# Kernel optimization log

Measured on AMD Instinct MI355X. Metric: run time of the kernel, lower is better.

The kernel has to match this reference:

```python
import jax, jax.numpy as jnp
import numpy as np

COST_COORDINATE = 1.0  # init kwarg cost_coordinate


def _lsa(cost):
    """Rectangular linear sum assignment (Jonker-Volgenant shortest augmenting
    path), matching scipy.optimize.linear_sum_assignment's algorithm/output.
    Returns (row_ind, col_ind) sorted by row_ind, length = min(nr, nc)."""
    cost = np.asarray(cost, dtype=np.float64)
    transposed = cost.shape[0] > cost.shape[1]
    if transposed:
        cost = cost.T
    nr, nc = cost.shape
    u = np.zeros(nr)
    v = np.zeros(nc)
    path = np.full(nc, -1, dtype=np.int64)
    col4row = np.full(nr, -1, dtype=np.int64)
    row4col = np.full(nc, -1, dtype=np.int64)
    for cur_row in range(nr):
        shortest = np.full(nc, np.inf)
        SR = np.zeros(nr, dtype=bool)
        SC = np.zeros(nc, dtype=bool)
        remaining = np.ones(nc, dtype=bool)
        min_val = 0.0
        i = cur_row
        sink = -1
        while sink == -1:
            SR[i] = True
            rem = np.nonzero(remaining)[0]
            cand = min_val + cost[i, rem] - u[i] - v[rem]
            better = cand < shortest[rem]
            idx_b = rem[better]
            shortest[idx_b] = cand[better]
            path[idx_b] = i
            j = rem[np.argmin(shortest[rem])]
            min_val = shortest[j]
            if not np.isfinite(min_val):
                raise RuntimeError('cost matrix is infeasible')
            SC[j] = True
            remaining[j] = False
            if row4col[j] == -1:
                sink = j
            else:
                i = row4col[j]
        # dual updates
        u[cur_row] += min_val
        mask = SR.copy()
        mask[cur_row] = False
        u[mask] += min_val - shortest[col4row[mask]]
        v[SC] -= min_val - shortest[SC]
        # augment along alternating path
        j = sink
        while True:
            i = path[j]
            row4col[j] = i
            col4row[i], j = j, col4row[i]
            if i == cur_row:
                break
    if transposed:
        order = np.argsort(col4row)
        return col4row[order], order.astype(np.int64)
    return np.arange(nr, dtype=np.int64), col4row


def setup_inputs() -> dict:
    key = jax.random.key(0)
    k1, k2 = jax.random.split(key)
    outputs = jax.random.uniform(k1, (16, 4096, 4), dtype=jnp.float32)  # [B, Q, 4]
    targets = jax.random.uniform(k2, (16, 128, 4), dtype=jnp.float32)   # [B, nt, 4]
    return {'outputs': outputs, 'targets': targets}


@jax.jit
def _cost_matrix(outputs, targets):
    # Block-diagonal part of torch.cdist(out.flatten(0,1), cat(targets), p=1):
    # only the per-image [Q, nt] blocks survive the .split(sizes, -1) in the
    # original, so we compute exactly those. C[b,q,t] = sum_d |out - tgt|.
    return COST_COORDINATE * jnp.abs(
        outputs[:, :, None, :] - targets[:, None, :, :]
    ).sum(-1)  # [B, Q, nt]


def reference(outputs, targets):
    C = _cost_matrix(outputs, targets)
    Cn = np.asarray(jax.device_get(C), dtype=np.float64)
    rows, cols = [], []
    for b in range(Cn.shape[0]):  # batch loop mirrors the original scipy loop
        r, c = _lsa(Cn[b])
        rows.append(r)
        cols.append(c)
    row_ind = jnp.asarray(np.stack(rows), dtype=jnp.int64)  # [B, min(Q,nt)]
    col_ind = jnp.asarray(np.stack(cols), dtype=jnp.int64)  # [B, min(Q,nt)]
    return C, row_ind, col_ind
```

## Files before the change

kernel.cpp:

```cpp
#include <hip/hip_runtime.h>
#include <math.h>

#define NB   16
#define NQ   4096
#define NTGT 128
#define CELEMS (NB * NQ * NTGT)

#define NSLOT 64
#define AT   512
#define ACPT 8
#define ANW  (AT / 64)

typedef unsigned long long u64;

__global__ __launch_bounds__(256) void cost_kernel(
    const float* __restrict__ outputs,
    const float* __restrict__ targets,
    float* __restrict__ C,
    u64*   __restrict__ rowkey2)
{
    __shared__ u64 part[4][NTGT];
    const int tid  = threadIdx.x;
    const int t4   = tid & 31;
    const int b    = blockIdx.x >> 6;
    const int blk  = blockIdx.x & (NSLOT - 1);
    const int idx0 = blockIdx.x * 2048 + tid;

    const float4* tg = reinterpret_cast<const float4*>(targets) + (b << 7) + (t4 << 2);
    float4 g[4];
    #pragma unroll
    for (int f = 0; f < 4; ++f) g[f] = tg[f];

    u64 keymin[4] = {~0ull, ~0ull, ~0ull, ~0ull};

    #pragma unroll
    for (int e = 0; e < 8; ++e) {
        int idx = idx0 + 256 * e;
        int bq  = idx >> 5;
        float4 o = reinterpret_cast<const float4*>(outputs)[bq];
        u64 q = (u64)(unsigned)(bq & (NQ - 1));
        float r[4];
        #pragma unroll
        for (int f = 0; f < 4; ++f) {
            float4 gg = g[f];
            r[f] = (fabsf(o.x - gg.x) + fabsf(o.y - gg.y)) +
                   (fabsf(o.z - gg.z) + fabsf(o.w - gg.w));
            u64 key = (((u64)__float_as_uint(r[f])) << 32) | q;
            if (key < keymin[f]) keymin[f] = key;
        }
        reinterpret_cast<float4*>(C)[idx] = make_float4(r[0], r[1], r[2], r[3]);
    }

    #pragma unroll
    for (int f = 0; f < 4; ++f) {
        u64 ov = __shfl_xor(keymin[f], 32);
        if (ov < keymin[f]) keymin[f] = ov;
    }
    if ((tid & 63) < 32) {
        int w = tid >> 6;
        #pragma unroll
        for (int f = 0; f < 4; ++f) part[w][(t4 << 2) + f] = keymin[f];
    }
    __syncthreads();

    if (tid < NTGT) {
        u64 k = part[0][tid];
        #pragma unroll
        for (int s = 1; s < 4; ++s) { u64 ov = part[s][tid]; if (ov < k) k = ov; }
        rowkey2[(((size_t)b * NSLOT) + blk) * NTGT + tid] = k;
    }
}

__global__ __launch_bounds__(AT, 1) void lsa_kernel(
    const float* __restrict__ outputs,
    const float* __restrict__ targets,
    const u64*   __restrict__ rowkey2,
    float* __restrict__ row_out,
    float* __restrict__ col_out)
{
    __shared__ double2 svp_[NQ];
    __shared__ unsigned claim_[NQ];
    __shared__ short  row4col_[NQ];
    __shared__ unsigned char path_[NQ];
    __shared__ float4 tgt_[NTGT];
    __shared__ double u_[NTGT];
    __shared__ u64    red2_[4][NTGT];
    __shared__ int    rowarg_[NTGT];
    __shared__ short  col4row_[NTGT];
    __shared__ short  left_[NTGT];
    __shared__ int    sc_j[NTGT];
    __shared__ double red_val[2][ANW];
    __shared__ int    red_idx[2][ANW];
    __shared__ u64    bmask_[2];

    const int tid = threadIdx.x;
    const int b   = blockIdx.x;
    const float4* outq = reinterpret_cast<const float4*>(outputs) + b * NQ;

    float4 o0 = outq[tid];
    float4 o1 = outq[tid + AT];
    float4 o2 = outq[tid + AT * 2];
    float4 o3 = outq[tid + AT * 3];
    float4 o4 = outq[tid + AT * 4];
    float4 o5 = outq[tid + AT * 5];
    float4 o6 = outq[tid + AT * 6];
    float4 o7 = outq[tid + AT * 7];

    #pragma unroll
    for (int kk = 0; kk < ACPT; ++kk) {
        int k = tid + AT * kk;
        svp_[k] = make_double2(0.0, 0.0);
        row4col_[k] = -1;
        claim_[k] = 0xFFFFFFFFu;
    }

    {
        const int t = tid & 127, s = tid >> 7;
        const u64* rk = rowkey2 + (size_t)b * NSLOT * NTGT;
        u64 k = ~0ull;
        #pragma unroll
        for (int gg = 0; gg < NSLOT / 4; ++gg) {
            u64 ov = rk[(s * (NSLOT / 4) + gg) * NTGT + t];
            if (ov < k) k = ov;
        }
        red2_[s][t] = k;
    }
    __syncthreads();

    if (tid < NTGT) {
        u64 key = red2_[0][tid];
        #pragma unroll
        for (int s = 1; s < 4; ++s) { u64 ov = red2_[s][tid]; if (ov < key) key = ov; }
        u_[tid] = (double)__uint_as_float((unsigned)(key >> 32));
        rowarg_[tid] = (int)(key & 0xffffffffu);
        tgt_[tid] = reinterpret_cast<const float4*>(targets)[b * NTGT + tid];
    }
    __syncthreads();

    if (tid < NTGT) atomicMin(&claim_[rowarg_[tid]], (unsigned)tid);
    __syncthreads();

    bool un = false;
    if (tid < NTGT) {
        int j = rowarg_[tid];
        bool won = (claim_[j] == (unsigned)tid);
        col4row_[tid] = won ? (short)j : (short)-1;
        if (won) row4col_[j] = (short)tid;
        un = !won;
    }
    {
        u64 m = __ballot(un);
        if ((tid & 63) == 0 && (tid >> 6) < 2) bmask_[tid >> 6] = m;
    }
    __syncthreads();
    const int nleft = __popcll(bmask_[0]) + __popcll(bmask_[1]);
    if (un) {
        int lane = tid & 63, w = tid >> 6;
        int r = __popcll(bmask_[w] & ((1ull << lane) - 1)) + (w ? __popcll(bmask_[0]) : 0);
        left_[r] = (short)tid;
    }
    __syncthreads();

    int parity = 0;

#define COSTN(g, on) ((fabsf((on).x - (g).x) + fabsf((on).y - (g).y)) + \
                      (fabsf((on).z - (g).z) + fabsf((on).w - (g).w)))

    for (int li = 0; li < nleft; ++li) {
        const int cur = left_[li];
        const int j0  = rowarg_[cur];
        const bool fast = (svp_[j0].y == 0.0);
        int      i;
        double   minv = 0.0;
        int      fj   = -1;
        int      Lns  = 0;
        unsigned rem  = 0xFFu;
        unsigned pend = 0u;
        bool     first = true;

        const double uc = u_[cur];
        const float4 gc = tgt_[cur];

        if (fast) {
            i = row4col_[j0];
            fj = j0; Lns = 1;
            if ((j0 & (AT - 1)) == tid) {
                rem  &= ~(1u << (j0 >> 9));
                pend |=  (1u << (j0 >> 9));
                svp_[j0].x = 0.0;
                path_[j0] = (unsigned char)cur;
            }
            if (tid == 0) sc_j[0] = j0;
        } else {
            i = cur;
        }

        while (true) {
            const double ui = u_[i];
            const float4 g  = tgt_[i];

            double bv = (double)INFINITY;
            int    bi = 0x7fffffff;

            if (first && fast) {
                #define FSTEP(n, on)                                            \
                {   int k = tid + AT * n;                                       \
                    double vk = svp_[k].y;                                      \
                    double cand_c = ((0.0 + (double)COSTN(gc, on)) - uc) - vk;  \
                    double cand_w = ((0.0 + (double)COSTN(g,  on)) - ui) - vk;  \
                    bool wless = cand_w < cand_c;                               \
                    double s = wless ? cand_w : cand_c;                         \
                    if ((rem >> n) & 1u) {                                      \
                        svp_[k].x = s;                                          \
                        path_[k] = (unsigned char)(wless ? i : cur);            \
                        if (s < bv) { bv = s; bi = k; }                         \
                    }                                                           \
                }
                FSTEP(0, o0) FSTEP(1, o1) FSTEP(2, o2) FSTEP(3, o3)
                FSTEP(4, o4) FSTEP(5, o5) FSTEP(6, o6) FSTEP(7, o7)
                #undef FSTEP
            } else if (first) {
                #define ISTEP(n, on)                                            \
                {   int k = tid + AT * n;                                       \
                    double vk = svp_[k].y;                                      \
                    double s = ((0.0 + (double)COSTN(gc, on)) - uc) - vk;       \
                    svp_[k].x = s;                                              \
                    path_[k] = (unsigned char)cur;                              \
                    if (s < bv) { bv = s; bi = k; }                             \
                }
                ISTEP(0, o0) ISTEP(1, o1) ISTEP(2, o2) ISTEP(3, o3)
                ISTEP(4, o4) ISTEP(5, o5) ISTEP(6, o6) ISTEP(7, o7)
                #undef ISTEP
            } else {
                #define USTEP(n, on)                                            \
                {   int k = tid + AT * n;                                       \
                    double2 sv = svp_[k];                                       \
                    double cand = ((minv + (double)COSTN(g, on)) - ui) - sv.y;  \
                    bool valid = (rem >> n) & 1u;                               \
                    double s = sv.x;                                            \
                    if (valid && cand < s) {                                    \
                        s = cand; svp_[k].x = cand;                             \
                        path_[k] = (unsigned char)i;                            \
                    }                                                           \
                    if (valid && s < bv) { bv = s; bi = k; }                    \
                }
                USTEP(0, o0) USTEP(1, o1) USTEP(2, o2) USTEP(3, o3)
                USTEP(4, o4) USTEP(5, o5) USTEP(6, o6) USTEP(7, o7)
                #undef USTEP
            }
            first = false;

            for (int off = 32; off > 0; off >>= 1) {
                double ov = __shfl_down(bv, off);
                int    oi = __shfl_down(bi, off);
                if (ov < bv || (ov == bv && oi < bi)) { bv = ov; bi = oi; }
            }
            if ((tid & 63) == 0) { red_val[parity][tid >> 6] = bv; red_idx[parity][tid >> 6] = bi; }
            __syncthreads();

            double fv = red_val[parity][0];
            int    jj = red_idx[parity][0];
            #pragma unroll
            for (int w = 1; w < ANW; ++w) {
                double ov = red_val[parity][w];
                int    oi = red_idx[parity][w];
                if (ov < fv || (ov == fv && oi < jj)) { fv = ov; jj = oi; }
            }
            parity ^= 1;

            fj   = jj;
            minv = fv;

            int r = row4col_[fj];
            if ((fj & (AT - 1)) == tid) {
                rem &= ~(1u << (fj >> 9));
                if (r >= 0) pend |= (1u << (fj >> 9));
            }
            if (r < 0) break;
            if (tid == 0) sc_j[Lns] = fj;
            Lns++;
            i = r;
        }

        const double dfin = minv;
        #pragma unroll
        for (int kk = 0; kk < ACPT; ++kk)
            if (pend & (1u << kk)) {
                int k = tid + AT * kk;
                svp_[k].y -= dfin - svp_[k].x;
            }
        if (tid == 0) {
            u_[cur] += dfin;
            for (int e = 0; e < Lns; ++e) {
                int j = sc_j[e];
                u_[row4col_[j]] += dfin - svp_[j].x;
            }
            int j = fj;
            while (true) {
                int i2 = path_[j];
                row4col_[j] = (short)i2;
                int nj = col4row_[i2];
                col4row_[i2] = (short)j;
                j = nj;
                if (i2 == cur) break;
            }
        }
        __syncthreads();
    }
#undef COSTN

    if (tid < NTGT) {
        int val = col4row_[tid];
        int rank = 0;
        #pragma unroll
        for (int k = 0; k < NTGT; ++k) rank += (col4row_[k] < val);
        row_out[b * NTGT + rank] = (float)val;
        col_out[b * NTGT + rank] = (float)tid;
    }
}

extern "C" void kernel_launch(void* const* d_in, const int* in_sizes, int n_in,
                              void* d_out, int out_size, void* d_ws, size_t ws_size,
                              hipStream_t stream) {
    const float* outputs = (const float*)d_in[0];
    const float* targets = (const float*)d_in[1];
    float* out = (float*)d_out;

    u64* rowkey2 = (u64*)d_ws;

    hipLaunchKernelGGL(cost_kernel, dim3(NB * NSLOT), dim3(256), 0, stream,
                       outputs, targets, out, rowkey2);
    hipLaunchKernelGGL(lsa_kernel, dim3(NB), dim3(AT), 0, stream,
                       outputs, targets, rowkey2,
                       out + CELEMS, out + CELEMS + NB * NTGT);
}
```

Before: 36.81 us.

## Move cost-matrix stores into LSA launch and pack argmin reduction keys

```diff
diff --git a/kernel.cpp b/kernel.cpp
--- a/kernel.cpp
+++ b/kernel.cpp
@@ -10,13 +10,13 @@
 #define AT   512
 #define ACPT 8
 #define ANW  (AT / 64)
+#define NCOST (CELEMS / 4 / 2048)
 
 typedef unsigned long long u64;
 
-__global__ __launch_bounds__(256) void cost_kernel(
+__global__ __launch_bounds__(256) void rowmin_kernel(
     const float* __restrict__ outputs,
     const float* __restrict__ targets,
-    float* __restrict__ C,
     u64*   __restrict__ rowkey2)
 {
     __shared__ u64 part[4][NTGT];
@@ -39,16 +39,14 @@
         int bq  = idx >> 5;
         float4 o = reinterpret_cast<const float4*>(outputs)[bq];
         u64 q = (u64)(unsigned)(bq & (NQ - 1));
-        float r[4];
         #pragma unroll
         for (int f = 0; f < 4; ++f) {
             float4 gg = g[f];
-            r[f] = (fabsf(o.x - gg.x) + fabsf(o.y - gg.y)) +
-                   (fabsf(o.z - gg.z) + fabsf(o.w - gg.w));
-            u64 key = (((u64)__float_as_uint(r[f])) << 32) | q;
+            float r = (fabsf(o.x - gg.x) + fabsf(o.y - gg.y)) +
+                      (fabsf(o.z - gg.z) + fabsf(o.w - gg.w));
+            u64 key = (((u64)__float_as_uint(r)) << 32) | q;
             if (key < keymin[f]) keymin[f] = key;
         }
-        reinterpret_cast<float4*>(C)[idx] = make_float4(r[0], r[1], r[2], r[3]);
     }
 
     #pragma unroll
@@ -71,10 +69,11 @@
     }
 }
 
-__global__ __launch_bounds__(AT, 1) void lsa_kernel(
+__global__ __launch_bounds__(AT, 1) void fused_kernel(
     const float* __restrict__ outputs,
     const float* __restrict__ targets,
     const u64*   __restrict__ rowkey2,
+    float* __restrict__ C,
     float* __restrict__ row_out,
     float* __restrict__ col_out)
 {
@@ -89,12 +88,37 @@
     __shared__ short  col4row_[NTGT];
     __shared__ short  left_[NTGT];
     __shared__ int    sc_j[NTGT];
-    __shared__ double red_val[2][ANW];
-    __shared__ int    red_idx[2][ANW];
+    __shared__ u64    redk_[2][ANW];
     __shared__ u64    bmask_[2];
 
     const int tid = threadIdx.x;
-    const int b   = blockIdx.x;
+
+    if (blockIdx.x >= NB) {
+        const int blk = blockIdx.x - NB;
+        const int t4  = tid & 31;
+        const float4* tg = reinterpret_cast<const float4*>(targets);
+        float4 g0, g1, g2, g3;
+        {
+            int b = (blk * 2048 + tid) >> 17;
+            const float4* tgb = tg + (b << 7) + (t4 << 2);
+            g0 = tgb[0]; g1 = tgb[1]; g2 = tgb[2]; g3 = tgb[3];
+        }
+        #pragma unroll
+        for (int e = 0; e < 4; ++e) {
+            int f  = blk * 2048 + e * 512 + tid;
+            int bq = f >> 5;
+            float4 o = reinterpret_cast<const float4*>(outputs)[bq];
+            float4 r;
+            r.x = (fabsf(o.x - g0.x) + fabsf(o.y - g0.y)) + (fabsf(o.z - g0.z) + fabsf(o.w - g0.w));
+            r.y = (fabsf(o.x - g1.x) + fabsf(o.y - g1.y)) + (fabsf(o.z - g1.z) + fabsf(o.w - g1.w));
+            r.z = (fabsf(o.x - g2.x) + fabsf(o.y - g2.y)) + (fabsf(o.z - g2.z) + fabsf(o.w - g2.w));
+            r.w = (fabsf(o.x - g3.x) + fabsf(o.y - g3.y)) + (fabsf(o.z - g3.z) + fabsf(o.w - g3.w));
+            reinterpret_cast<float4*>(C)[f] = r;
+        }
+        return;
+    }
+
+    const int b = blockIdx.x;
     const float4* outq = reinterpret_cast<const float4*>(outputs) + b * NQ;
 
     float4 o0 = outq[tid];
@@ -200,7 +224,7 @@
             const float4 g  = tgt_[i];
 
             double bv = (double)INFINITY;
-            int    bi = 0x7fffffff;
+            int    bi = 0xFFF;
 
             if (first && fast) {
                 #define FSTEP(n, on)                                            \
@@ -250,26 +274,25 @@
             }
             first = false;
 
+            u64 key = (__double_as_longlong(bv) & ~0xFFFull) | (unsigned)bi;
+            #pragma unroll
             for (int off = 32; off > 0; off >>= 1) {
-                double ov = __shfl_down(bv, off);
-                int    oi = __shfl_down(bi, off);
-                if (ov < bv || (ov == bv && oi < bi)) { bv = ov; bi = oi; }
-            }
-            if ((tid & 63) == 0) { red_val[parity][tid >> 6] = bv; red_idx[parity][tid >> 6] = bi; }
+                u64 ok = __shfl_down(key, off);
+                if (ok < key) key = ok;
+            }
+            if ((tid & 63) == 0) redk_[parity][tid >> 6] = key;
             __syncthreads();
 
-            double fv = red_val[parity][0];
-            int    jj = red_idx[parity][0];
+            u64 fkey = redk_[parity][0];
             #pragma unroll
             for (int w = 1; w < ANW; ++w) {
-                double ov = red_val[parity][w];
-                int    oi = red_idx[parity][w];
-                if (ov < fv || (ov == fv && oi < jj)) { fv = ov; jj = oi; }
+                u64 ok = redk_[parity][w];
+                if (ok < fkey) fkey = ok;
             }
             parity ^= 1;
 
-            fj   = jj;
-            minv = fv;
+            fj   = (int)(fkey & 0xFFFull);
+            minv = __longlong_as_double((long long)(fkey & ~0xFFFull));
 
             int r = row4col_[fj];
             if ((fj & (AT - 1)) == tid) {
@@ -328,9 +351,9 @@
 
     u64* rowkey2 = (u64*)d_ws;
 
-    hipLaunchKernelGGL(cost_kernel, dim3(NB * NSLOT), dim3(256), 0, stream,
-                       outputs, targets, out, rowkey2);
-    hipLaunchKernelGGL(lsa_kernel, dim3(NB), dim3(AT), 0, stream,
-                       outputs, targets, rowkey2,
+    hipLaunchKernelGGL(rowmin_kernel, dim3(NB * NSLOT), dim3(256), 0, stream,
+                       outputs, targets, rowkey2);
+    hipLaunchKernelGGL(fused_kernel, dim3(NB + NCOST), dim3(AT), 0, stream,
+                       outputs, targets, rowkey2, out,
                        out + CELEMS, out + CELEMS + NB * NTGT);
 }
```

After: 31.72 us. 1.16x faster.
